# Optimization experiments

Measured on AMD Instinct MI355X. Metric: run time of the kernel, lower is better.

## Reference

```python
import jax, jax.numpy as jnp
import numpy as np

B = 65536
IMG = 9            # input spatial size; conv 2x2 valid -> 8x8 = 64 features
RBF_IN = 64
RBF_OUT = 16
HID = 32
GAMMA = 1.0
THRESHOLD = 0.0


def setup_inputs() -> dict:
    key = jax.random.key(0)
    ks = jax.random.split(key, 8)
    x = jax.random.normal(ks[0], (B, 1, IMG, IMG), dtype=jnp.float32)
    conv_w = jax.random.normal(ks[1], (1, 1, 2, 2), dtype=jnp.float32) * 0.5
    conv_b = jax.random.normal(ks[2], (1,), dtype=jnp.float32) * 0.1
    centers = jax.random.normal(ks[3], (RBF_OUT, RBF_IN), dtype=jnp.float32)
    w1 = jax.random.normal(ks[4], (RBF_OUT, HID), dtype=jnp.float32) * (1.0 / np.sqrt(RBF_OUT))
    b1 = jnp.zeros((HID,), dtype=jnp.float32)
    w2 = jax.random.normal(ks[5], (HID, 1), dtype=jnp.float32) * (1.0 / np.sqrt(HID))
    b2 = jnp.zeros((1,), dtype=jnp.float32)
    return {"x": x, "conv_w": conv_w, "conv_b": conv_b, "centers": centers,
            "w1": w1, "b1": b1, "w2": w2, "b2": b2}


def reference(x, conv_w, conv_b, centers, w1, b1, w2, b2):
    # ConvFilter: 2x2 valid conv + bias, sigmoid(logits - threshold)
    logits = jax.lax.conv_general_dilated(
        x, conv_w, window_strides=(1, 1), padding="VALID",
        dimension_numbers=("NCHW", "OIHW", "NCHW"))
    logits = logits + conv_b[None, :, None, None]
    act = jax.nn.sigmoid(logits - THRESHOLD)          # [B,1,8,8]
    flat = act.reshape(act.shape[0], -1)               # [B,64]
    # RBFLayer: exp(-gamma * ||x - c||^2), broadcast diff [B,16,64]
    diff = flat[:, None, :] - centers[None, :, :]
    dist_sq = jnp.sum(diff * diff, axis=-1)            # [B,16]
    rbf = jnp.exp(-GAMMA * dist_sq)
    # Classifier: Linear(16,32) -> tanh -> Linear(32,1) -> sigmoid -> squeeze
    h = jnp.tanh(rbf @ w1 + b1)
    out = jax.nn.sigmoid(h @ w2 + b2)
    return out.squeeze(-1)                              # [B]
```

## Files before the change

### kernel.cpp

```cpp
#include <hip/hip_runtime.h>


constexpr int NPIX    = 81;
constexpr int RBF_IN  = 64;
constexpr int RBF_OUT = 16;
constexpr int HID     = 32;

__device__ __forceinline__ float sigmoid_f(float v) {
    return __builtin_amdgcn_rcpf(1.0f + __expf(-v));
}

__device__ __forceinline__ float tanh_f(float v) {
    float vc = fminf(fmaxf(v, -15.0f), 15.0f);
    float e  = __expf(2.0f * vc);
    return (e - 1.0f) * __builtin_amdgcn_rcpf(e + 1.0f);
}

__global__ __launch_bounds__(256, 1) void qcnn_fused(
    const float* __restrict__ x,
    const float* __restrict__ conv_w,
    const float* __restrict__ conv_b,
    const float* __restrict__ centers,
    const float* __restrict__ w1,
    const float* __restrict__ b1,
    const float* __restrict__ w2,
    const float* __restrict__ b2,
    float* __restrict__ out,
    int nB)
{
    __shared__ float s_c2t[RBF_IN * RBF_OUT];
    __shared__ float s_cc[RBF_OUT];
    __shared__ float s_w1t[HID * RBF_OUT];
    __shared__ float s_b1[HID];
    __shared__ float s_w2[HID];

    const int tid = threadIdx.x;
    for (int idx = tid; idx < RBF_IN * RBF_OUT; idx += 256) {
        int k = idx >> 4, j = idx & 15;
        s_c2t[idx] = -2.0f * centers[j * RBF_IN + k];
    }
    for (int idx = tid; idx < HID * RBF_OUT; idx += 256) {
        int i = idx >> 4, j = idx & 15;
        s_w1t[idx] = w1[j * HID + i];
    }
    if (tid < HID) { s_b1[tid] = b1[tid]; s_w2[tid] = w2[tid]; }
    if (tid < RBF_OUT) {
        float s = 0.0f;
        for (int k = 0; k < RBF_IN; ++k) {
            float c = centers[tid * RBF_IN + k];
            s = fmaf(c, c, s);
        }
        s_cc[tid] = s;
    }
    __syncthreads();

    const int b = blockIdx.x * 256 + tid;
    if (b >= nB) return;

    const float w00 = conv_w[0], w01 = conv_w[1], w10 = conv_w[2], w11 = conv_w[3];
    const float cbias = conv_b[0];

    const float* __restrict__ xp = x + (size_t)b * NPIX;
    float xr[NPIX];
    #pragma unroll
    for (int i = 0; i < NPIX; ++i) xr[i] = xp[i];

    float dot[RBF_OUT];
    #pragma unroll
    for (int j = 0; j < RBF_OUT; ++j) dot[j] = 0.0f;
    float S2 = 0.0f;

    #pragma unroll
    for (int r = 0; r < 8; ++r) {
        #pragma unroll
        for (int c = 0; c < 8; ++c) {
            float v = cbias;
            v = fmaf(w00, xr[r*9 + c],      v);
            v = fmaf(w01, xr[r*9 + c + 1],  v);
            v = fmaf(w10, xr[r*9 + 9 + c],  v);
            v = fmaf(w11, xr[r*9 + 10 + c], v);
            float a = sigmoid_f(v);
            S2 = fmaf(a, a, S2);
            const int k = r*8 + c;
            #pragma unroll
            for (int j = 0; j < RBF_OUT; ++j)
                dot[j] = fmaf(a, s_c2t[k*RBF_OUT + j], dot[j]);
        }
    }

    float rbf[RBF_OUT];
    #pragma unroll
    for (int j = 0; j < RBF_OUT; ++j)
        rbf[j] = __expf(-(S2 + dot[j] + s_cc[j]));

    float acc = b2[0];
    #pragma unroll
    for (int i = 0; i < HID; ++i) {
        float hv = s_b1[i];
        #pragma unroll
        for (int j = 0; j < RBF_OUT; ++j)
            hv = fmaf(rbf[j], s_w1t[i*RBF_OUT + j], hv);
        acc = fmaf(tanh_f(hv), s_w2[i], acc);
    }
    out[b] = sigmoid_f(acc);
}

extern "C" void kernel_launch(void* const* d_in, const int* in_sizes, int n_in,
                              void* d_out, int out_size, void* d_ws, size_t ws_size,
                              hipStream_t stream) {
    const float* x       = (const float*)d_in[0];
    const float* conv_w  = (const float*)d_in[1];
    const float* conv_b  = (const float*)d_in[2];
    const float* centers = (const float*)d_in[3];
    const float* w1      = (const float*)d_in[4];
    const float* b1      = (const float*)d_in[5];
    const float* w2      = (const float*)d_in[6];
    const float* b2      = (const float*)d_in[7];
    float* out = (float*)d_out;

    int nB = out_size;
    int grid = (nB + 255) / 256;
    qcnn_fused<<<grid, 256, 0, stream>>>(x, conv_w, conv_b, centers,
                                         w1, b1, w2, b2, out, nB);
}
```

Before: 87.86 us.

## Stage input rows through LDS with coalesced float4 loads, halve block size

```diff
diff --git a/kernel.cpp b/kernel.cpp
--- a/kernel.cpp
+++ b/kernel.cpp
@@ -5,6 +5,7 @@
 constexpr int RBF_IN  = 64;
 constexpr int RBF_OUT = 16;
 constexpr int HID     = 32;
+constexpr int SPB     = 128;
 
 __device__ __forceinline__ float sigmoid_f(float v) {
     return __builtin_amdgcn_rcpf(1.0f + __expf(-v));
@@ -16,7 +17,7 @@
     return (e - 1.0f) * __builtin_amdgcn_rcpf(e + 1.0f);
 }
 
-__global__ __launch_bounds__(256, 1) void qcnn_fused(
+__global__ __launch_bounds__(SPB, 1) void qcnn_fused(
     const float* __restrict__ x,
     const float* __restrict__ conv_w,
     const float* __restrict__ conv_b,
@@ -28,6 +29,7 @@
     float* __restrict__ out,
     int nB)
 {
+    __shared__ float s_x[SPB * NPIX];
     __shared__ float s_c2t[RBF_IN * RBF_OUT];
     __shared__ float s_cc[RBF_OUT];
     __shared__ float s_w1t[HID * RBF_OUT];
@@ -35,11 +37,33 @@
     __shared__ float s_w2[HID];
 
     const int tid = threadIdx.x;
-    for (int idx = tid; idx < RBF_IN * RBF_OUT; idx += 256) {
+
+    {
+        const size_t base  = (size_t)blockIdx.x * (SPB * NPIX);
+        const size_t total = (size_t)nB * NPIX;
+        if (base + (size_t)(SPB * NPIX) <= total) {
+            const float4* __restrict__ xv = (const float4*)(x + base);
+            float4* sv = (float4*)s_x;
+            #pragma unroll
+            for (int i = 0; i < (SPB * NPIX / 4) / SPB; ++i)
+                sv[i * SPB + tid] = xv[i * SPB + tid];
+            {
+                int i = 20 * SPB + tid;
+                if (i < SPB * NPIX / 4) sv[i] = xv[i];
+            }
+        } else {
+            for (int i = tid; i < SPB * NPIX; i += SPB) {
+                size_t g = base + i;
+                s_x[i] = (g < total) ? x[g] : 0.0f;
+            }
+        }
+    }
+
+    for (int idx = tid; idx < RBF_IN * RBF_OUT; idx += SPB) {
         int k = idx >> 4, j = idx & 15;
         s_c2t[idx] = -2.0f * centers[j * RBF_IN + k];
     }
-    for (int idx = tid; idx < HID * RBF_OUT; idx += 256) {
+    for (int idx = tid; idx < HID * RBF_OUT; idx += SPB) {
         int i = idx >> 4, j = idx & 15;
         s_w1t[idx] = w1[j * HID + i];
     }
@@ -54,16 +78,16 @@
     }
     __syncthreads();
 
-    const int b = blockIdx.x * 256 + tid;
+    const int b = blockIdx.x * SPB + tid;
     if (b >= nB) return;
 
     const float w00 = conv_w[0], w01 = conv_w[1], w10 = conv_w[2], w11 = conv_w[3];
     const float cbias = conv_b[0];
 
-    const float* __restrict__ xp = x + (size_t)b * NPIX;
+    const float* __restrict__ row = &s_x[tid * NPIX];
     float xr[NPIX];
     #pragma unroll
-    for (int i = 0; i < NPIX; ++i) xr[i] = xp[i];
+    for (int i = 0; i < NPIX; ++i) xr[i] = row[i];
 
     float dot[RBF_OUT];
     #pragma unroll
@@ -119,7 +143,7 @@
     float* out = (float*)d_out;
 
     int nB = out_size;
-    int grid = (nB + 255) / 256;
-    qcnn_fused<<<grid, 256, 0, stream>>>(x, conv_w, conv_b, centers,
+    int grid = (nB + SPB - 1) / SPB;
+    qcnn_fused<<<grid, SPB, 0, stream>>>(x, conv_w, conv_b, centers,
                                          w1, b1, w2, b2, out, nB);
 }
```

After: 90.60 us. 3.1% more time.
